# Performance work log

Hardware: AMD Instinct MI355X
Metric: run time of the kernel (lower is better)

## Reference

```python
import jax, jax.numpy as jnp
import numpy as np

BATCH = 16384
NUM_INPUTS = 128
# features = squares (n) + singles (n) + pairs C(n,2)
NUM_FEATS = NUM_INPUTS + NUM_INPUTS + (NUM_INPUTS * (NUM_INPUTS - 1)) // 2  # 8384

# precompute pair index lists (equivalent to itertools.combinations(range(n), 2))
_II, _JJ = np.triu_indices(NUM_INPUTS, k=1)
_II = jnp.asarray(_II)
_JJ = jnp.asarray(_JJ)


def setup_inputs() -> dict:
    key = jax.random.key(0)
    k1, k2 = jax.random.split(key)
    x = jax.random.normal(k1, (BATCH, NUM_INPUTS), dtype=jnp.float32)
    w = jax.random.normal(k2, (NUM_FEATS,), dtype=jnp.float32) * 0.05
    return {"x": x, "w": w}


def reference(x, w):
    # order=2, with_squares=True
    # squares block: o=1 -> inputs**2 / 1**2
    sq = x * x
    # combination order 1: f = 1! -> x / 1
    singles = x
    # combination order 2: f = 2! -> x_i * x_j / 2 for all i<j (combinations order)
    pairs = (x[:, _II] * x[:, _JJ]) * jnp.float32(0.5)
    t = jnp.concatenate([sq, singles, pairs], axis=-1)  # [B, 8384]
    return t * w
```

## Files before the change

### kernel.cpp

```cpp
#include <hip/hip_runtime.h>


constexpr int BATCH = 16384;
constexpr int NIN   = 128;
constexpr int NFEAT = NIN + NIN + (NIN * (NIN - 1)) / 2;
constexpr int BROWS = 32;
constexpr int TPB   = 256;

__device__ __forceinline__ int pair_off(int i) {
    return i * (NIN - 1) - (i * (i - 1)) / 2;
}

__global__ __launch_bounds__(TPB) void cpl_kernel(const float* __restrict__ x,
                                                  const float* __restrict__ w,
                                                  float* __restrict__ out) {
    __shared__ float xs[BROWS * NIN];

    const int tid = threadIdx.x;
    const int b0  = blockIdx.y * BROWS;

    {
        const float4* src = reinterpret_cast<const float4*>(x + (size_t)b0 * NIN);
        float4*       dst = reinterpret_cast<float4*>(xs);
#pragma unroll
        for (int k = 0; k < (BROWS * NIN / 4) / TPB; ++k)
            dst[k * TPB + tid] = src[k * TPB + tid];
    }
    __syncthreads();

    const int f = blockIdx.x * TPB + tid;
    if (f >= NFEAT) return;

    int i1, i2, mode;
    if (f < NIN) {
        i1 = f; i2 = f; mode = 0;
    } else if (f < 2 * NIN) {
        i1 = f - NIN; i2 = f - NIN; mode = 1;
    } else {
        const int p = f - 2 * NIN;
        float s = sqrtf((float)(65025 - 8 * p));
        int   i = (int)((255.0f - s) * 0.5f);
        i = min(max(i, 0), NIN - 2);
        while (pair_off(i + 1) <= p) ++i;
        while (pair_off(i) > p)      --i;
        i1 = i;
        i2 = i + 1 + (p - pair_off(i));
        mode = 2;
    }
    const float wf = w[f];

    float* op = out + (size_t)b0 * NFEAT + f;
#pragma unroll
    for (int b = 0; b < BROWS; ++b) {
        const float xi = xs[b * NIN + i1];
        const float xj = xs[b * NIN + i2];
        float p = xi * xj;
        if (mode == 1) p = xi;
        if (mode == 2) p *= 0.5f;
        op[(size_t)b * NFEAT] = p * wf;
    }
}

extern "C" void kernel_launch(void* const* d_in, const int* in_sizes, int n_in,
                              void* d_out, int out_size, void* d_ws, size_t ws_size,
                              hipStream_t stream) {
    const float* x = (const float*)d_in[0];
    const float* w = (const float*)d_in[1];
    float*     out = (float*)d_out;

    dim3 block(TPB);
    dim3 grid((NFEAT + TPB - 1) / TPB,
              BATCH / BROWS);
    cpl_kernel<<<grid, block, 0, stream>>>(x, w, out);
}
```

Before: 101.7 us.

## Use persistent blocks that loop over row tiles with register-prefetched x and a separate tail

```diff
diff --git a/kernel.cpp b/kernel.cpp
--- a/kernel.cpp
+++ b/kernel.cpp
@@ -3,61 +3,97 @@
 
 constexpr int BATCH = 16384;
 constexpr int NIN   = 128;
-constexpr int NFEAT = NIN + NIN + (NIN * (NIN - 1)) / 2;
+constexpr int NFEAT = 2 * NIN + NIN * (NIN - 1) / 2;
+constexpr int TPB   = 256;
 constexpr int BROWS = 32;
-constexpr int TPB   = 256;
+constexpr int NWIN  = 32;
+constexpr int FMAIN = NWIN * TPB;
+constexpr int NTAIL = NFEAT - FMAIN;
+constexpr int NBY   = 64;
+constexpr int NT    = 8;
+constexpr int NBLK  = NWIN * NBY;
 
-__device__ __forceinline__ int pair_off(int i) {
-    return i * (NIN - 1) - (i * (i - 1)) / 2;
+__device__ __forceinline__ int pair_off(int i) { return i * (NIN - 1) - (i * (i - 1)) / 2; }
+
+__device__ __forceinline__ void decode_pair(int p, int& i, int& j) {
+    float s = sqrtf((float)(65025 - 8 * p));
+    int  ii = (int)((255.0f - s) * 0.5f);
+    ii = min(max(ii, 0), NIN - 2);
+    while (pair_off(ii + 1) <= p) ++ii;
+    while (pair_off(ii)     >  p) --ii;
+    i = ii; j = ii + 1 + (p - pair_off(ii));
 }
 
 __global__ __launch_bounds__(TPB) void cpl_kernel(const float* __restrict__ x,
                                                   const float* __restrict__ w,
                                                   float* __restrict__ out) {
     __shared__ float xs[BROWS * NIN];
+    const int tid = threadIdx.x;
+    const int wid = blockIdx.x;
+    const int bx  = wid & (NWIN - 1);
+    const int by  = wid >> 5;
 
-    const int tid = threadIdx.x;
-    const int b0  = blockIdx.y * BROWS;
+    const int f = bx * TPB + tid;
+    int i1, i2, mode;
+    if (f < NIN)          { i1 = f;       i2 = f;  mode = 0; }
+    else if (f < 2 * NIN) { i1 = f - NIN; i2 = i1; mode = 1; }
+    else                  { decode_pair(f - 2 * NIN, i1, i2); mode = 2; }
+    const float wf = w[f];
 
+    const float4* xv = reinterpret_cast<const float4*>(x);
+    float4 p0, p1, p2, p3;
     {
-        const float4* src = reinterpret_cast<const float4*>(x + (size_t)b0 * NIN);
-        float4*       dst = reinterpret_cast<float4*>(xs);
+        const size_t s0 = (size_t)by * BROWS * (NIN / 4);
+        p0 = xv[s0 + 0 * TPB + tid];
+        p1 = xv[s0 + 1 * TPB + tid];
+        p2 = xv[s0 + 2 * TPB + tid];
+        p3 = xv[s0 + 3 * TPB + tid];
+    }
+
 #pragma unroll
-        for (int k = 0; k < (BROWS * NIN / 4) / TPB; ++k)
-            dst[k * TPB + tid] = src[k * TPB + tid];
+    for (int q = 0; q < 6; ++q) {
+        const int e  = q * TPB + tid;
+        const int r  = wid * 8 + e / NTAIL;
+        const int ft = FMAIN + e % NTAIL;
+        int ti, tj; decode_pair(ft - 2 * NIN, ti, tj);
+        const float xi = x[(size_t)r * NIN + ti];
+        const float xj = x[(size_t)r * NIN + tj];
+        float p = xi * xj; p *= 0.5f;
+        out[(size_t)r * NFEAT + ft] = p * w[ft];
     }
+
+    float4* xsv = reinterpret_cast<float4*>(xs);
+    xsv[0 * TPB + tid] = p0; xsv[1 * TPB + tid] = p1;
+    xsv[2 * TPB + tid] = p2; xsv[3 * TPB + tid] = p3;
     __syncthreads();
 
-    const int f = blockIdx.x * TPB + tid;
-    if (f >= NFEAT) return;
+    for (int k = 0; k < NT; ++k) {
+        if (k + 1 < NT) {
+            const size_t sn = (size_t)(by + NBY * (k + 1)) * BROWS * (NIN / 4);
+            p0 = xv[sn + 0 * TPB + tid];
+            p1 = xv[sn + 1 * TPB + tid];
+            p2 = xv[sn + 2 * TPB + tid];
+            p3 = xv[sn + 3 * TPB + tid];
+        }
 
-    int i1, i2, mode;
-    if (f < NIN) {
-        i1 = f; i2 = f; mode = 0;
-    } else if (f < 2 * NIN) {
-        i1 = f - NIN; i2 = f - NIN; mode = 1;
-    } else {
-        const int p = f - 2 * NIN;
-        float s = sqrtf((float)(65025 - 8 * p));
-        int   i = (int)((255.0f - s) * 0.5f);
-        i = min(max(i, 0), NIN - 2);
-        while (pair_off(i + 1) <= p) ++i;
-        while (pair_off(i) > p)      --i;
-        i1 = i;
-        i2 = i + 1 + (p - pair_off(i));
-        mode = 2;
-    }
-    const float wf = w[f];
+        const int rg = by + NBY * k;
+        float* op = out + (size_t)rg * BROWS * NFEAT + f;
+#pragma unroll
+        for (int b = 0; b < BROWS; ++b) {
+            const float xi = xs[b * NIN + i1];
+            const float xj = xs[b * NIN + i2];
+            float p = xi * xj;
+            if (mode == 1) p = xi;
+            if (mode == 2) p *= 0.5f;
+            op[(size_t)b * NFEAT] = p * wf;
+        }
 
-    float* op = out + (size_t)b0 * NFEAT + f;
-#pragma unroll
-    for (int b = 0; b < BROWS; ++b) {
-        const float xi = xs[b * NIN + i1];
-        const float xj = xs[b * NIN + i2];
-        float p = xi * xj;
-        if (mode == 1) p = xi;
-        if (mode == 2) p *= 0.5f;
-        op[(size_t)b * NFEAT] = p * wf;
+        if (k + 1 < NT) {
+            __syncthreads();
+            xsv[0 * TPB + tid] = p0; xsv[1 * TPB + tid] = p1;
+            xsv[2 * TPB + tid] = p2; xsv[3 * TPB + tid] = p3;
+            __syncthreads();
+        }
     }
 }
 
@@ -68,8 +104,5 @@
     const float* w = (const float*)d_in[1];
     float*     out = (float*)d_out;
 
-    dim3 block(TPB);
-    dim3 grid((NFEAT + TPB - 1) / TPB,
-              BATCH / BROWS);
-    cpl_kernel<<<grid, block, 0, stream>>>(x, w, out);
+    cpl_kernel<<<dim3(NBLK), dim3(TPB), 0, stream>>>(x, w, out);
 }
```

Result: slower. 114.3 us (+12.4%).
